# Kernel tuning notes

Measured on AMD Instinct MI355X. Metric: run time of the kernel, lower is better.

The kernel has to match this reference:

```python
import jax, jax.numpy as jnp
import numpy as np

EPS = 1e-08
LN_EPS = 1e-05


def _layernorm(x, g, b):
    mu = jnp.mean(x, axis=-1, keepdims=True)
    var = jnp.var(x, axis=-1, keepdims=True)
    return (x - mu) * jax.lax.rsqrt(var + LN_EPS) * g + b


def _prob(x):
    x = jnp.tanh(x) * 0.499 + 0.5
    return jnp.clip(x / (jnp.sum(x, axis=-1, keepdims=True) + EPS), EPS)


def setup_inputs() -> dict:
    key = jax.random.key(0)
    ks = jax.random.split(key, 8)
    B, N, D = 8, 2048, 1024
    H = 4 * D
    s = 0.02
    return {
        'q': jax.random.normal(ks[0], (B, N, D), jnp.float32),
        'k': jax.random.normal(ks[1], (B, N, D), jnp.float32),
        'v': jax.random.normal(ks[2], (B, N, D), jnp.float32),
        'W_diff': jax.random.normal(ks[3], (D, D), jnp.float32) * s,
        'b_diff': jnp.zeros((D,), jnp.float32),
        'ln_g': jnp.ones((D,), jnp.float32),
        'ln_b': jnp.zeros((D,), jnp.float32),
        'W1': jax.random.normal(ks[4], (H, D), jnp.float32) * s,
        'b1': jnp.zeros((H,), jnp.float32),
        'W2': jax.random.normal(ks[5], (D, H), jnp.float32) * s,
        'b2': jnp.zeros((D,), jnp.float32),
    }


def reference(q, k, v, W_diff, b_diff, ln_g, ln_b, W1, b1, W2, b2):
    D = q.shape[-1]
    q_prob = _prob(q)  # [B,N,D]
    k_prob = _prob(k)  # [B,N,D]
    log_ratio = jnp.log(q_prob) - jnp.log(k_prob)  # [B,N,D]
    # sid[b,i,j] = sum_d (q_prob[b,i,d] - k_prob[b,i,d]) * log_ratio[b,j,d]
    sid = jnp.einsum('bnd,bmd->bnm', q_prob - k_prob, log_ratio)
    sid_sim = -sid
    attn = jax.nn.softmax(sid_sim / (D ** 0.5), axis=-1)  # [B,N,N]
    attn_feat = jnp.einsum('bnm,bmd->bnd', attn, v)
    f_diff = (v - attn_feat) @ W_diff.T + b_diff + q
    h = _layernorm(f_diff, ln_g, ln_b)
    mlp = jax.nn.gelu(h @ W1.T + b1, approximate=False) @ W2.T + b2
    out = mlp + f_diff
    return _layernorm(out, ln_g, ln_b)
```

## Files before the change

### kernel.cpp

```cpp
#include <hip/hip_runtime.h>
#include <math.h>

typedef unsigned short u16;
typedef __attribute__((ext_vector_type(4))) unsigned short u16x4;
typedef __attribute__((ext_vector_type(8))) short s16x8;
typedef __attribute__((ext_vector_type(4))) float f32x4;
typedef __attribute__((ext_vector_type(4))) float f4v;

#define DEVI static __device__ __forceinline__

DEVI u16 f2bf(float f) {
  union { float f; unsigned u; } c; c.f = f;
  return (u16)((c.u + 0x7FFFu + ((c.u >> 16) & 1u)) >> 16);
}
DEVI float bf2f(u16 h) {
  union { unsigned u; float f; } c; c.u = ((unsigned)h) << 16;
  return c.f;
}
DEVI unsigned cvt_pk_bf16(float lo, float hi) {
  unsigned r;
  asm("v_cvt_pk_bf16_f32 %0, %1, %2" : "=v"(r) : "v"(lo), "v"(hi));
  return r;
}

DEVI float tanh_fast(float x) {
  float e = __expf(2.0f * x);
  float r = __builtin_amdgcn_rcpf(e + 1.0f);
  return fmaf(-2.0f, r, 1.0f);
}
DEVI float gelu_fast(float x) {
  float x2 = x * x;
  float u = x * fmaf(x2, 0.0356774081f, 0.7978845608f);
  float e = __expf(2.0f * u);
  float r = __builtin_amdgcn_rcpf(e + 1.0f);
  float t = fmaf(-2.0f, r, 1.0f);
  float hx = 0.5f * x;
  return fmaf(hx, t, hx);
}

DEVI void load_lds16(const u16* g, u16* l) {
  __builtin_amdgcn_global_load_lds(
      (const __attribute__((address_space(1))) void*)g,
      (__attribute__((address_space(3))) void*)l, 16, 0, 0);
}

#define BARL()                                                             \
  asm volatile("s_barrier\n\ts_waitcnt lgkmcnt(0)" ::: "memory");          \
  __builtin_amdgcn_sched_barrier(0)
#define BARL_VM4()                                                         \
  asm volatile("s_waitcnt vmcnt(4)\n\ts_barrier\n\ts_waitcnt lgkmcnt(0)" ::: "memory"); \
  __builtin_amdgcn_sched_barrier(0)
#define BARL_VM0()                                                         \
  asm volatile("s_waitcnt vmcnt(0)\n\ts_barrier\n\ts_waitcnt lgkmcnt(0)" ::: "memory"); \
  __builtin_amdgcn_sched_barrier(0)


__global__ __launch_bounds__(256) void cast3_kernel(
    const float* __restrict__ wd, const float* __restrict__ w1,
    const float* __restrict__ w2, u16* __restrict__ owd,
    u16* __restrict__ ow1, u16* __restrict__ ow2) {
  const int n1 = 262144, n2 = 1048576;
  int i = blockIdx.x * 256 + threadIdx.x;
  const float* src; u16* dst; int j;
  if (i < n1) { src = wd; dst = owd; j = i; }
  else if (i < n1 + n2) { src = w1; dst = ow1; j = i - n1; }
  else { src = w2; dst = ow2; j = i - n1 - n2; }
  f4v f = ((const f4v*)src)[j];
  u16x4 o;
  o[0] = f2bf(f[0]); o[1] = f2bf(f[1]); o[2] = f2bf(f[2]); o[3] = f2bf(f[3]);
  ((u16x4*)dst)[j] = o;
}

__global__ __launch_bounds__(256) void prob_kernel(
    const float* __restrict__ q, const float* __restrict__ k,
    u16* __restrict__ A, u16* __restrict__ Bm) {
  const int D = 1024;
  size_t row = blockIdx.x;
  int t = threadIdx.x;
  f4v qv = ((const f4v*)(q + row * D))[t];
  f4v kv = ((const f4v*)(k + row * D))[t];
  float tq[4], tk[4];
  float sq = 0.f, sk = 0.f;
#pragma unroll
  for (int i = 0; i < 4; i++) {
    tq[i] = tanh_fast(qv[i]) * 0.499f + 0.5f;
    tk[i] = tanh_fast(kv[i]) * 0.499f + 0.5f;
    sq += tq[i]; sk += tk[i];
  }
#pragma unroll
  for (int off = 32; off > 0; off >>= 1) {
    sq += __shfl_xor(sq, off);
    sk += __shfl_xor(sk, off);
  }
  __shared__ float sbq[4], sbk[4];
  int lane = t & 63, w = t >> 6;
  if (lane == 0) { sbq[w] = sq; sbk[w] = sk; }
  __syncthreads();
  sq = sbq[0] + sbq[1] + sbq[2] + sbq[3];
  sk = sbk[0] + sbk[1] + sbk[2] + sbk[3];
  float iq = 1.0f / (sq + 1e-8f), ik = 1.0f / (sk + 1e-8f);
  u16x4 av, bv;
#pragma unroll
  for (int i = 0; i < 4; i++) {
    float qp = fmaxf(tq[i] * iq, 1e-8f);
    float kp = fmaxf(tk[i] * ik, 1e-8f);
    av[i] = f2bf(qp - kp);
    bv[i] = f2bf(__logf(qp) - __logf(kp));
  }
  ((u16x4*)(A + row * D))[t] = av;
  ((u16x4*)(Bm + row * D))[t] = bv;
}

__global__ __launch_bounds__(256) void transpose_v_kernel(
    const float* __restrict__ v, u16* __restrict__ Vt) {
  const int N = 2048, D = 1024;
  __shared__ float tile[32][33];
  int b = blockIdx.z;
  int d0 = blockIdx.x * 32, n0 = blockIdx.y * 32;
  int tx = threadIdx.x & 31, ty = threadIdx.x >> 5;
  const float* vb = v + (size_t)b * N * D;
  u16* vtb = Vt + (size_t)b * N * D;
#pragma unroll
  for (int i = 0; i < 4; i++)
    tile[ty + i * 8][tx] = vb[(size_t)(n0 + ty + i * 8) * D + d0 + tx];
  __syncthreads();
#pragma unroll
  for (int i = 0; i < 4; i++)
    vtb[(size_t)(d0 + ty + i * 8) * N + n0 + tx] = f2bf(tile[tx][ty + i * 8]);
}

__global__ __launch_bounds__(256) void softmax_rows_kernel(u16* __restrict__ S) {
  const int NN = 2048;
  size_t row = blockIdx.x;
  u16* r = S + row * NN;
  int t = threadIdx.x;
  s16x8 vv = ((const s16x8*)r)[t];
  float x[8];
  float mx = -1e30f;
#pragma unroll
  for (int i = 0; i < 8; i++) { x[i] = bf2f((u16)vv[i]); mx = fmaxf(mx, x[i]); }
#pragma unroll
  for (int off = 32; off > 0; off >>= 1) mx = fmaxf(mx, __shfl_xor(mx, off));
  __shared__ float sm[4], ss[4];
  int lane = t & 63, w = t >> 6;
  if (lane == 0) sm[w] = mx;
  __syncthreads();
  mx = fmaxf(fmaxf(sm[0], sm[1]), fmaxf(sm[2], sm[3]));
  float sum = 0.f;
#pragma unroll
  for (int i = 0; i < 8; i++) { x[i] = __expf(x[i] - mx); sum += x[i]; }
#pragma unroll
  for (int off = 32; off > 0; off >>= 1) sum += __shfl_xor(sum, off);
  if (lane == 0) ss[w] = sum;
  __syncthreads();
  float inv = 1.0f / (ss[0] + ss[1] + ss[2] + ss[3]);
  s16x8 ov;
#pragma unroll
  for (int i = 0; i < 8; i++) ov[i] = (short)f2bf(x[i] * inv);
  ((s16x8*)r)[t] = ov;
}

template <int IN_BF16, int OUT_BF16>
__global__ __launch_bounds__(256) void layernorm_rows_kernel(
    const void* __restrict__ inp, void* __restrict__ outp,
    const float* __restrict__ g, const float* __restrict__ bia) {
  const int D = 1024;
  size_t row = blockIdx.x;
  int t = threadIdx.x;
  f4v xv;
  if (IN_BF16) {
    u16x4 h4 = ((const u16x4*)inp)[row * (D / 4) + t];
    xv[0] = bf2f(h4[0]); xv[1] = bf2f(h4[1]); xv[2] = bf2f(h4[2]); xv[3] = bf2f(h4[3]);
  } else {
    xv = ((const f4v*)inp)[row * (D / 4) + t];
  }
  float s = xv[0] + xv[1] + xv[2] + xv[3];
  float s2 = xv[0] * xv[0] + xv[1] * xv[1] + xv[2] * xv[2] + xv[3] * xv[3];
#pragma unroll
  for (int off = 32; off > 0; off >>= 1) {
    s += __shfl_xor(s, off);
    s2 += __shfl_xor(s2, off);
  }
  __shared__ float sa[4], sb[4];
  int lane = t & 63, w = t >> 6;
  if (lane == 0) { sa[w] = s; sb[w] = s2; }
  __syncthreads();
  s = sa[0] + sa[1] + sa[2] + sa[3];
  s2 = sb[0] + sb[1] + sb[2] + sb[3];
  float mean = s * (1.0f / D);
  float var = s2 * (1.0f / D) - mean * mean;
  float rs = rsqrtf(var + 1e-5f);
  f4v gv = ((const f4v*)g)[t];
  f4v bv = ((const f4v*)bia)[t];
  float y[4];
#pragma unroll
  for (int i = 0; i < 4; i++) y[i] = (xv[i] - mean) * rs * gv[i] + bv[i];
  if (OUT_BF16) {
    u16x4 o; o[0] = f2bf(y[0]); o[1] = f2bf(y[1]); o[2] = f2bf(y[2]); o[3] = f2bf(y[3]);
    ((u16x4*)outp)[row * (D / 4) + t] = o;
  } else {
    f4v o; o[0] = y[0]; o[1] = y[1]; o[2] = y[2]; o[3] = y[3];
    ((f4v*)outp)[row * (D / 4) + t] = o;
  }
}

template <int EPI>
__global__ __launch_bounds__(512, 2) void gemm8_kernel(
    const u16* __restrict__ Ab, const u16* __restrict__ Bb,
    void* __restrict__ Cout,
    const float* __restrict__ aux1, const float* __restrict__ aux2,
    int M, int Nc, int K,
    long sA, long sB, long sC, long sAux1, float scale) {
  __shared__ u16 lds[65536];

  int nwg = gridDim.x;
  int orig = blockIdx.x;
  int swz = (orig & 7) * (nwg >> 3) + (orig >> 3);
  int gxm = M >> 8, gyn = Nc >> 8;
  int pb = gxm * gyn;
  int bz = swz / pb;
  int rem = swz - bz * pb;
  int gsz = gyn << 3;
  int gid = rem / gsz;
  int lr = rem - gid * gsz;
  int bx = (gid << 3) + (lr & 7);
  int by = lr >> 3;
  int m0 = bx << 8, n0 = by << 8;

  const u16* Ap = Ab + (size_t)bz * sA;
  const u16* Bp = Bb + (size_t)bz * sB;

  int t = threadIdx.x, wid = t >> 6, l = t & 63;
  int wr = wid >> 2, wc = wid & 3;
  int sr = l >> 3;
  int scb = ((l & 7) ^ sr) * 8;
  int frow = l & 15, fq = l >> 4, fx = l & 7;

  const size_t rowoff = (size_t)(wid * 16 + sr) * K + scb;
  const u16* pA0 = Ap + (size_t)m0 * K + rowoff;
  const u16* pA0h = pA0 + (size_t)8 * K;
  const u16* pA1 = pA0 + (size_t)128 * K;
  const u16* pA1h = pA1 + (size_t)8 * K;
  const u16* pB0 = Bp + (size_t)n0 * K + rowoff;
  const u16* pB0h = pB0 + (size_t)8 * K;
  const u16* pB1 = pB0 + (size_t)128 * K;
  const u16* pB1h = pB1 + (size_t)8 * K;
  u16* ldA = &lds[wid * 1024];
  u16* ldB = ldA + 32768;

  int aoffs[4][2], boffs[2][2];
#pragma unroll
  for (int m = 0; m < 4; m++)
#pragma unroll
    for (int kk = 0; kk < 2; kk++)
      aoffs[m][kk] = ((wr * 64 + m * 16 + frow) * 64 + ((kk * 4 + fq) ^ fx) * 8) * 2;
#pragma unroll
  for (int n = 0; n < 2; n++)
#pragma unroll
    for (int kk = 0; kk < 2; kk++)
      boffs[n][kk] = ((wc * 32 + n * 16 + frow) * 64 + ((kk * 4 + fq) ^ fx) * 8) * 2 + 65536;

  s16x8 af[4][2], bf0[2][2], bf1[2][2];
  auto rdA = [&](int sl, int h) {
#pragma unroll
    for (int m = 0; m < 4; m++)
#pragma unroll
      for (int kk = 0; kk < 2; kk++)
        af[m][kk] = *(const s16x8*)((const char*)lds +
                                    (aoffs[m][kk] + (sl * 32768 + h * 16384)));
  };
  auto rdB = [&](int sl, int h, s16x8 (&bf)[2][2]) {
#pragma unroll
    for (int n = 0; n < 2; n++)
#pragma unroll
      for (int kk = 0; kk < 2; kk++)
        bf[n][kk] = *(const s16x8*)((const char*)lds +
                                    (boffs[n][kk] + (sl * 32768 + h * 16384)));
  };

  f32x4 acc[2][2][4][2];
#pragma unroll
  for (int a = 0; a < 2; a++)
#pragma unroll
    for (int b = 0; b < 2; b++)
#pragma unroll
      for (int m = 0; m < 4; m++)
#pragma unroll
        for (int n = 0; n < 2; n++) acc[a][b][m][n] = (f32x4){0.f, 0.f, 0.f, 0.f};

#define MFMA_Q(QM, QN, BF)                                                    \
  do {                                                                        \
    __builtin_amdgcn_s_setprio(1);                                            \
    _Pragma("unroll") for (int m = 0; m < 4; m++)                             \
        _Pragma("unroll") for (int n = 0; n < 2; n++)                         \
        _Pragma("unroll") for (int kk = 0; kk < 2; kk++)                      \
            acc[QM][QN][m][n] = __builtin_amdgcn_mfma_f32_16x16x32_bf16(      \
                af[m][kk], BF[n][kk], acc[QM][QN][m][n], 0, 0, 0);            \
    __builtin_amdgcn_s_setprio(0);                                            \
  } while (0)

  load_lds16(pA0, ldA);              load_lds16(pA0h, ldA + 512);
  load_lds16(pB1, ldB + 8192);       load_lds16(pB1h, ldB + 8192 + 512);
  load_lds16(pB0, ldB);              load_lds16(pB0h, ldB + 512);
  load_lds16(pA1, ldA + 8192);       load_lds16(pA1h, ldA + 8192 + 512);
  load_lds16(pA0 + 64, ldA + 16384); load_lds16(pA0h + 64, ldA + 16384 + 512);
  load_lds16(pB1 + 64, ldB + 16384 + 8192);
  load_lds16(pB1h + 64, ldB + 16384 + 8192 + 512);
  asm volatile("s_waitcnt vmcnt(4)\n\ts_barrier" ::: "memory");

  int nt = K >> 6, niter = nt >> 1;
  for (int i = 0; i < niter - 1; i++) {
    rdA(0, 0); rdB(0, 0, bf0);
    load_lds16(pB0 + 64, ldB + 16384);
    load_lds16(pB0h + 64, ldB + 16384 + 512);
    BARL(); MFMA_Q(0, 0, bf0);
    rdB(0, 1, bf1);
    load_lds16(pA1 + 64, ldA + 16384 + 8192);
    load_lds16(pA1h + 64, ldA + 16384 + 8192 + 512);
    BARL(); MFMA_Q(0, 1, bf1);
    rdA(0, 1);
    load_lds16(pA0 + 128, ldA);
    load_lds16(pA0h + 128, ldA + 512);
    BARL(); MFMA_Q(1, 1, bf1);
    load_lds16(pB1 + 128, ldB + 8192);
    load_lds16(pB1h + 128, ldB + 8192 + 512);
    BARL_VM4(); MFMA_Q(1, 0, bf0);
    rdA(1, 0); rdB(1, 0, bf0);
    load_lds16(pB0 + 128, ldB);
    load_lds16(pB0h + 128, ldB + 512);
    BARL(); MFMA_Q(0, 0, bf0);
    rdB(1, 1, bf1);
    load_lds16(pA1 + 128, ldA + 8192);
    load_lds16(pA1h + 128, ldA + 8192 + 512);
    BARL(); MFMA_Q(0, 1, bf1);
    rdA(1, 1);
    load_lds16(pA0 + 192, ldA + 16384);
    load_lds16(pA0h + 192, ldA + 16384 + 512);
    BARL(); MFMA_Q(1, 1, bf1);
    load_lds16(pB1 + 192, ldB + 16384 + 8192);
    load_lds16(pB1h + 192, ldB + 16384 + 8192 + 512);
    BARL_VM4(); MFMA_Q(1, 0, bf0);
    pA0 += 128; pA0h += 128; pA1 += 128; pA1h += 128;
    pB0 += 128; pB0h += 128; pB1 += 128; pB1h += 128;
  }
  {
    rdA(0, 0); rdB(0, 0, bf0);
    load_lds16(pB0 + 64, ldB + 16384);
    load_lds16(pB0h + 64, ldB + 16384 + 512);
    BARL(); MFMA_Q(0, 0, bf0);
    rdB(0, 1, bf1);
    load_lds16(pA1 + 64, ldA + 16384 + 8192);
    load_lds16(pA1h + 64, ldA + 16384 + 8192 + 512);
    BARL(); MFMA_Q(0, 1, bf1);
    rdA(0, 1);
    BARL(); MFMA_Q(1, 1, bf1);
    BARL_VM0(); MFMA_Q(1, 0, bf0);
    rdA(1, 0); rdB(1, 0, bf0);
    MFMA_Q(0, 0, bf0);
    rdB(1, 1, bf1);
    MFMA_Q(0, 1, bf1);
    rdA(1, 1);
    MFMA_Q(1, 1, bf1);
    MFMA_Q(1, 0, bf0);
  }
#undef MFMA_Q

#pragma unroll
  for (int qm = 0; qm < 2; qm++) {
#pragma unroll
    for (int qn = 0; qn < 2; qn++) {
#pragma unroll
      for (int m = 0; m < 4; m++) {
#pragma unroll
        for (int n = 0; n < 2; n++) {
          f32x4 a4 = acc[qm][qn][m][n];
          int gcol = n0 + qn * 128 + wc * 32 + n * 16 + frow;
#pragma unroll
          for (int rp = 0; rp < 2; rp++) {
            int grow0 = m0 + qm * 128 + wr * 64 + m * 16 + fq * 4 + rp * 2;
            size_t ci0 = (size_t)grow0 * Nc + gcol;
            if (EPI == 0) {
              unsigned pk = cvt_pk_bf16(a4[rp * 2] * scale, a4[rp * 2 + 1] * scale);
              ((u16*)Cout)[(size_t)bz * sC + ci0] = (u16)pk;
              ((u16*)Cout)[(size_t)bz * sC + ci0 + Nc] = (u16)(pk >> 16);
            } else if (EPI == 1) {
              float v0 = aux1[(size_t)bz * sAux1 + ci0];
              float v1 = aux1[(size_t)bz * sAux1 + ci0 + Nc];
              unsigned pk = cvt_pk_bf16(v0 - a4[rp * 2], v1 - a4[rp * 2 + 1]);
              ((u16*)Cout)[(size_t)bz * sC + ci0] = (u16)pk;
              ((u16*)Cout)[(size_t)bz * sC + ci0 + Nc] = (u16)(pk >> 16);
            } else if (EPI == 3) {
              float b2v = aux2[gcol];
              unsigned pk = cvt_pk_bf16(gelu_fast(a4[rp * 2] + b2v),
                                        gelu_fast(a4[rp * 2 + 1] + b2v));
              ((u16*)Cout)[ci0] = (u16)pk;
              ((u16*)Cout)[ci0 + Nc] = (u16)(pk >> 16);
            } else if (EPI == 6) {
              float b2v = aux2[gcol];
              unsigned pk = cvt_pk_bf16(a4[rp * 2] + b2v + aux1[ci0],
                                        a4[rp * 2 + 1] + b2v + aux1[ci0 + Nc]);
              ((u16*)Cout)[ci0] = (u16)pk;
              ((u16*)Cout)[ci0 + Nc] = (u16)(pk >> 16);
            } else {
              float b2v = aux2[gcol];
              const u16* r16 = (const u16*)aux1;
              unsigned pk = cvt_pk_bf16(a4[rp * 2] + b2v + bf2f(r16[ci0]),
                                        a4[rp * 2 + 1] + b2v + bf2f(r16[ci0 + Nc]));
              ((u16*)Cout)[ci0] = (u16)pk;
              ((u16*)Cout)[ci0 + Nc] = (u16)(pk >> 16);
            }
          }
        }
      }
    }
  }
}


extern "C" void kernel_launch(void* const* d_in, const int* in_sizes, int n_in,
                              void* d_out, int out_size, void* d_ws, size_t ws_size,
                              hipStream_t stream) {
  const float* q      = (const float*)d_in[0];
  const float* k      = (const float*)d_in[1];
  const float* v      = (const float*)d_in[2];
  const float* W_diff = (const float*)d_in[3];
  const float* b_diff = (const float*)d_in[4];
  const float* ln_g   = (const float*)d_in[5];
  const float* ln_b   = (const float*)d_in[6];
  const float* W1     = (const float*)d_in[7];
  const float* b1     = (const float*)d_in[8];
  const float* W2     = (const float*)d_in[9];
  const float* b2     = (const float*)d_in[10];

  const int B = 8, N = 2048, D = 1024, H = 4096;
  char* ws = (char*)d_ws;
  u16* A    = (u16*)(ws + 0);
  u16* Bm   = (u16*)(ws + 33554432);
  u16* X    = (u16*)(ws + 33554432);
  u16* Vt   = (u16*)(ws + 67108864);
  u16* S    = (u16*)(ws + 100663296);
  u16* Hbf  = (u16*)(ws + 134217728);
  u16* Wd   = (u16*)(ws + 167772160);
  u16* W1b  = (u16*)(ws + 169869312);
  u16* W2b  = (u16*)(ws + 178257920);
  u16* G    = (u16*)(ws + 0);
  u16* Fbf  = (u16*)d_out;
  float* out = (float*)d_out;

  cast3_kernel<<<9216, 256, 0, stream>>>(W_diff, W1, W2, Wd, W1b, W2b);

  prob_kernel<<<B * N, 256, 0, stream>>>(q, k, A, Bm);
  transpose_v_kernel<<<dim3(D / 32, N / 32, B), 256, 0, stream>>>(v, Vt);

  gemm8_kernel<0><<<8 * 8 * 8, 512, 0, stream>>>(
      A, Bm, S, nullptr, nullptr, N, N, D,
      (long)N * D, (long)N * D, (long)N * N, 0, -0.03125f);

  softmax_rows_kernel<<<B * N, 256, 0, stream>>>(S);

  gemm8_kernel<1><<<8 * 4 * 8, 512, 0, stream>>>(
      S, Vt, X, v, nullptr, N, D, N,
      (long)N * N, (long)D * N, (long)N * D, (long)N * D, 1.0f);

  gemm8_kernel<6><<<64 * 4, 512, 0, stream>>>(
      X, Wd, Fbf, q, b_diff, B * N, D, D, 0, 0, 0, 0, 1.0f);

  layernorm_rows_kernel<1, 1><<<B * N, 256, 0, stream>>>(Fbf, Hbf, ln_g, ln_b);

  gemm8_kernel<3><<<64 * 16, 512, 0, stream>>>(
      Hbf, W1b, G, nullptr, b1, B * N, H, D, 0, 0, 0, 0, 1.0f);

  gemm8_kernel<7><<<64 * 4, 512, 0, stream>>>(
      G, W2b, Hbf, (const float*)Fbf, b2, B * N, D, H, 0, 0, 0, 0, 1.0f);

  layernorm_rows_kernel<1, 0><<<B * N, 256, 0, stream>>>(Hbf, out, ln_g, ln_b);
}
```

Before: 552.4 us.

## Rework GEMM to 256x128 tiles with 3-stage K=32 LDS pipeline

Replaces the 256x256 tile, 128-K-step hand-scheduled quadrant pipeline with a 256x128 output tile and a three-slot ring buffer of K=32 stages. LDS use drops to about 72KB per block and launch bounds request four blocks per CU, with one barrier per K step. Grid sizes double to match. The aim is higher occupancy and simpler latency hiding. The cost is less operand reuse per tile (more global and LDS traffic per FLOP), plus more barriers per unit of work because each K step is shorter.

```diff
diff --git a/kernel.cpp b/kernel.cpp
--- a/kernel.cpp
+++ b/kernel.cpp
@@ -44,14 +44,10 @@
       (__attribute__((address_space(3))) void*)l, 16, 0, 0);
 }
 
-#define BARL()                                                             \
-  asm volatile("s_barrier\n\ts_waitcnt lgkmcnt(0)" ::: "memory");          \
-  __builtin_amdgcn_sched_barrier(0)
-#define BARL_VM4()                                                         \
-  asm volatile("s_waitcnt vmcnt(4)\n\ts_barrier\n\ts_waitcnt lgkmcnt(0)" ::: "memory"); \
-  __builtin_amdgcn_sched_barrier(0)
-#define BARL_VM0()                                                         \
-  asm volatile("s_waitcnt vmcnt(0)\n\ts_barrier\n\ts_waitcnt lgkmcnt(0)" ::: "memory"); \
+#define SYNC_VM3() asm volatile("s_waitcnt vmcnt(3)\n\ts_barrier" ::: "memory")
+#define SYNC_VM0() asm volatile("s_waitcnt vmcnt(0)\n\ts_barrier" ::: "memory")
+#define LGKM0()                                                \
+  asm volatile("s_waitcnt lgkmcnt(0)" ::: "memory");           \
   __builtin_amdgcn_sched_barrier(0)
 
 
@@ -205,18 +201,18 @@
 }
 
 template <int EPI>
-__global__ __launch_bounds__(512, 2) void gemm8_kernel(
+__global__ __launch_bounds__(512, 4) void gemm8_kernel(
     const u16* __restrict__ Ab, const u16* __restrict__ Bb,
     void* __restrict__ Cout,
     const float* __restrict__ aux1, const float* __restrict__ aux2,
     int M, int Nc, int K,
     long sA, long sB, long sC, long sAux1, float scale) {
-  __shared__ u16 lds[65536];
+  __shared__ u16 lds[36864];
 
   int nwg = gridDim.x;
   int orig = blockIdx.x;
   int swz = (orig & 7) * (nwg >> 3) + (orig >> 3);
-  int gxm = M >> 8, gyn = Nc >> 8;
+  int gxm = M >> 8, gyn = Nc >> 7;
   int pb = gxm * gyn;
   int bz = swz / pb;
   int rem = swz - bz * pb;
@@ -225,191 +221,134 @@
   int lr = rem - gid * gsz;
   int bx = (gid << 3) + (lr & 7);
   int by = lr >> 3;
-  int m0 = bx << 8, n0 = by << 8;
+  int m0 = bx << 8, n0 = by << 7;
 
   const u16* Ap = Ab + (size_t)bz * sA;
   const u16* Bp = Bb + (size_t)bz * sB;
 
   int t = threadIdx.x, wid = t >> 6, l = t & 63;
-  int wr = wid >> 2, wc = wid & 3;
-  int sr = l >> 3;
-  int scb = ((l & 7) ^ sr) * 8;
-  int frow = l & 15, fq = l >> 4, fx = l & 7;
-
-  const size_t rowoff = (size_t)(wid * 16 + sr) * K + scb;
-  const u16* pA0 = Ap + (size_t)m0 * K + rowoff;
-  const u16* pA0h = pA0 + (size_t)8 * K;
+  int wr = wid >> 1, wc = wid & 1;
+  int frow = l & 15, fq = l >> 4;
+
+  int srow = t >> 2;
+  int scg = ((t & 3) ^ ((t >> 3) & 3)) * 8;
+  const u16* pB  = Bp + ((size_t)n0 + srow) * K + scg;
+  const u16* pA0 = Ap + ((size_t)m0 + srow) * K + scg;
   const u16* pA1 = pA0 + (size_t)128 * K;
-  const u16* pA1h = pA1 + (size_t)8 * K;
-  const u16* pB0 = Bp + (size_t)n0 * K + rowoff;
-  const u16* pB0h = pB0 + (size_t)8 * K;
-  const u16* pB1 = pB0 + (size_t)128 * K;
-  const u16* pB1h = pB1 + (size_t)8 * K;
-  u16* ldA = &lds[wid * 1024];
-  u16* ldB = ldA + 32768;
-
-  int aoffs[4][2], boffs[2][2];
+
+  int aoffs[4], boffs[4];
+  int abase = (wr >> 1) * 8192;
+#pragma unroll
+  for (int m = 0; m < 4; m++) {
+    int rh = (wr & 1) * 64 + m * 16 + frow;
+    aoffs[m] = abase + rh * 64 + ((fq ^ ((rh >> 1) & 3)) * 16);
+  }
+#pragma unroll
+  for (int n = 0; n < 4; n++) {
+    int rb = wc * 64 + n * 16 + frow;
+    boffs[n] = 16384 + rb * 64 + ((fq ^ ((rb >> 1) & 3)) * 16);
+  }
+
+  s16x8 af[4], bf[4];
+  auto rdAB = [&](int slotB) {
+#pragma unroll
+    for (int m = 0; m < 4; m++)
+      af[m] = *(const s16x8*)((const char*)lds + (aoffs[m] + slotB));
+#pragma unroll
+    for (int n = 0; n < 4; n++)
+      bf[n] = *(const s16x8*)((const char*)lds + (boffs[n] + slotB));
+  };
+  auto stage = [&](int slotU16, const u16* b, const u16* a0, const u16* a1) {
+    load_lds16(b,  &lds[slotU16 + 8192 + t * 8]);
+    load_lds16(a0, &lds[slotU16 + t * 8]);
+    load_lds16(a1, &lds[slotU16 + 4096 + t * 8]);
+  };
+
+  f32x4 acc[4][4];
 #pragma unroll
   for (int m = 0; m < 4; m++)
 #pragma unroll
-    for (int kk = 0; kk < 2; kk++)
-      aoffs[m][kk] = ((wr * 64 + m * 16 + frow) * 64 + ((kk * 4 + fq) ^ fx) * 8) * 2;
-#pragma unroll
-  for (int n = 0; n < 2; n++)
-#pragma unroll
-    for (int kk = 0; kk < 2; kk++)
-      boffs[n][kk] = ((wc * 32 + n * 16 + frow) * 64 + ((kk * 4 + fq) ^ fx) * 8) * 2 + 65536;
-
-  s16x8 af[4][2], bf0[2][2], bf1[2][2];
-  auto rdA = [&](int sl, int h) {
-#pragma unroll
-    for (int m = 0; m < 4; m++)
-#pragma unroll
-      for (int kk = 0; kk < 2; kk++)
-        af[m][kk] = *(const s16x8*)((const char*)lds +
-                                    (aoffs[m][kk] + (sl * 32768 + h * 16384)));
-  };
-  auto rdB = [&](int sl, int h, s16x8 (&bf)[2][2]) {
-#pragma unroll
-    for (int n = 0; n < 2; n++)
-#pragma unroll
-      for (int kk = 0; kk < 2; kk++)
-        bf[n][kk] = *(const s16x8*)((const char*)lds +
-                                    (boffs[n][kk] + (sl * 32768 + h * 16384)));
-  };
-
-  f32x4 acc[2][2][4][2];
-#pragma unroll
-  for (int a = 0; a < 2; a++)
-#pragma unroll
-    for (int b = 0; b < 2; b++)
-#pragma unroll
-      for (int m = 0; m < 4; m++)
-#pragma unroll
-        for (int n = 0; n < 2; n++) acc[a][b][m][n] = (f32x4){0.f, 0.f, 0.f, 0.f};
-
-#define MFMA_Q(QM, QN, BF)                                                    \
+    for (int n = 0; n < 4; n++) acc[m][n] = (f32x4){0.f, 0.f, 0.f, 0.f};
+
+#define MFMA_ALL()                                                            \
   do {                                                                        \
     __builtin_amdgcn_s_setprio(1);                                            \
     _Pragma("unroll") for (int m = 0; m < 4; m++)                             \
-        _Pragma("unroll") for (int n = 0; n < 2; n++)                         \
-        _Pragma("unroll") for (int kk = 0; kk < 2; kk++)                      \
-            acc[QM][QN][m][n] = __builtin_amdgcn_mfma_f32_16x16x32_bf16(      \
-                af[m][kk], BF[n][kk], acc[QM][QN][m][n], 0, 0, 0);            \
+        _Pragma("unroll") for (int n = 0; n < 4; n++)                         \
+            acc[m][n] = __builtin_amdgcn_mfma_f32_16x16x32_bf16(              \
+                af[m], bf[n], acc[m][n], 0, 0, 0);                            \
     __builtin_amdgcn_s_setprio(0);                                            \
   } while (0)
 
-  load_lds16(pA0, ldA);              load_lds16(pA0h, ldA + 512);
-  load_lds16(pB1, ldB + 8192);       load_lds16(pB1h, ldB + 8192 + 512);
-  load_lds16(pB0, ldB);              load_lds16(pB0h, ldB + 512);
-  load_lds16(pA1, ldA + 8192);       load_lds16(pA1h, ldA + 8192 + 512);
-  load_lds16(pA0 + 64, ldA + 16384); load_lds16(pA0h + 64, ldA + 16384 + 512);
-  load_lds16(pB1 + 64, ldB + 16384 + 8192);
-  load_lds16(pB1h + 64, ldB + 16384 + 8192 + 512);
-  asm volatile("s_waitcnt vmcnt(4)\n\ts_barrier" ::: "memory");
-
-  int nt = K >> 6, niter = nt >> 1;
-  for (int i = 0; i < niter - 1; i++) {
-    rdA(0, 0); rdB(0, 0, bf0);
-    load_lds16(pB0 + 64, ldB + 16384);
-    load_lds16(pB0h + 64, ldB + 16384 + 512);
-    BARL(); MFMA_Q(0, 0, bf0);
-    rdB(0, 1, bf1);
-    load_lds16(pA1 + 64, ldA + 16384 + 8192);
-    load_lds16(pA1h + 64, ldA + 16384 + 8192 + 512);
-    BARL(); MFMA_Q(0, 1, bf1);
-    rdA(0, 1);
-    load_lds16(pA0 + 128, ldA);
-    load_lds16(pA0h + 128, ldA + 512);
-    BARL(); MFMA_Q(1, 1, bf1);
-    load_lds16(pB1 + 128, ldB + 8192);
-    load_lds16(pB1h + 128, ldB + 8192 + 512);
-    BARL_VM4(); MFMA_Q(1, 0, bf0);
-    rdA(1, 0); rdB(1, 0, bf0);
-    load_lds16(pB0 + 128, ldB);
-    load_lds16(pB0h + 128, ldB + 512);
-    BARL(); MFMA_Q(0, 0, bf0);
-    rdB(1, 1, bf1);
-    load_lds16(pA1 + 128, ldA + 8192);
-    load_lds16(pA1h + 128, ldA + 8192 + 512);
-    BARL(); MFMA_Q(0, 1, bf1);
-    rdA(1, 1);
-    load_lds16(pA0 + 192, ldA + 16384);
-    load_lds16(pA0h + 192, ldA + 16384 + 512);
-    BARL(); MFMA_Q(1, 1, bf1);
-    load_lds16(pB1 + 192, ldB + 16384 + 8192);
-    load_lds16(pB1h + 192, ldB + 16384 + 8192 + 512);
-    BARL_VM4(); MFMA_Q(1, 0, bf0);
-    pA0 += 128; pA0h += 128; pA1 += 128; pA1h += 128;
-    pB0 += 128; pB0h += 128; pB1 += 128; pB1h += 128;
-  }
-  {
-    rdA(0, 0); rdB(0, 0, bf0);
-    load_lds16(pB0 + 64, ldB + 16384);
-    load_lds16(pB0h + 64, ldB + 16384 + 512);
-    BARL(); MFMA_Q(0, 0, bf0);
-    rdB(0, 1, bf1);
-    load_lds16(pA1 + 64, ldA + 16384 + 8192);
-    load_lds16(pA1h + 64, ldA + 16384 + 8192 + 512);
-    BARL(); MFMA_Q(0, 1, bf1);
-    rdA(0, 1);
-    BARL(); MFMA_Q(1, 1, bf1);
-    BARL_VM0(); MFMA_Q(1, 0, bf0);
-    rdA(1, 0); rdB(1, 0, bf0);
-    MFMA_Q(0, 0, bf0);
-    rdB(1, 1, bf1);
-    MFMA_Q(0, 1, bf1);
-    rdA(1, 1);
-    MFMA_Q(1, 1, bf1);
-    MFMA_Q(1, 0, bf0);
-  }
-#undef MFMA_Q
-
-#pragma unroll
-  for (int qm = 0; qm < 2; qm++) {
-#pragma unroll
-    for (int qn = 0; qn < 2; qn++) {
-#pragma unroll
-      for (int m = 0; m < 4; m++) {
-#pragma unroll
-        for (int n = 0; n < 2; n++) {
-          f32x4 a4 = acc[qm][qn][m][n];
-          int gcol = n0 + qn * 128 + wc * 32 + n * 16 + frow;
-#pragma unroll
-          for (int rp = 0; rp < 2; rp++) {
-            int grow0 = m0 + qm * 128 + wr * 64 + m * 16 + fq * 4 + rp * 2;
-            size_t ci0 = (size_t)grow0 * Nc + gcol;
-            if (EPI == 0) {
-              unsigned pk = cvt_pk_bf16(a4[rp * 2] * scale, a4[rp * 2 + 1] * scale);
-              ((u16*)Cout)[(size_t)bz * sC + ci0] = (u16)pk;
-              ((u16*)Cout)[(size_t)bz * sC + ci0 + Nc] = (u16)(pk >> 16);
-            } else if (EPI == 1) {
-              float v0 = aux1[(size_t)bz * sAux1 + ci0];
-              float v1 = aux1[(size_t)bz * sAux1 + ci0 + Nc];
-              unsigned pk = cvt_pk_bf16(v0 - a4[rp * 2], v1 - a4[rp * 2 + 1]);
-              ((u16*)Cout)[(size_t)bz * sC + ci0] = (u16)pk;
-              ((u16*)Cout)[(size_t)bz * sC + ci0 + Nc] = (u16)(pk >> 16);
-            } else if (EPI == 3) {
-              float b2v = aux2[gcol];
-              unsigned pk = cvt_pk_bf16(gelu_fast(a4[rp * 2] + b2v),
-                                        gelu_fast(a4[rp * 2 + 1] + b2v));
-              ((u16*)Cout)[ci0] = (u16)pk;
-              ((u16*)Cout)[ci0 + Nc] = (u16)(pk >> 16);
-            } else if (EPI == 6) {
-              float b2v = aux2[gcol];
-              unsigned pk = cvt_pk_bf16(a4[rp * 2] + b2v + aux1[ci0],
-                                        a4[rp * 2 + 1] + b2v + aux1[ci0 + Nc]);
-              ((u16*)Cout)[ci0] = (u16)pk;
-              ((u16*)Cout)[ci0 + Nc] = (u16)(pk >> 16);
-            } else {
-              float b2v = aux2[gcol];
-              const u16* r16 = (const u16*)aux1;
-              unsigned pk = cvt_pk_bf16(a4[rp * 2] + b2v + bf2f(r16[ci0]),
-                                        a4[rp * 2 + 1] + b2v + bf2f(r16[ci0 + Nc]));
-              ((u16*)Cout)[ci0] = (u16)pk;
-              ((u16*)Cout)[ci0 + Nc] = (u16)(pk >> 16);
-            }
-          }
+  stage(0, pB, pA0, pA1);
+  stage(12288, pB + 32, pA0 + 32, pA1 + 32);
+
+  int nt = K >> 5;
+  int cur = 0;
+  int stg = 24576;
+  const u16* gB  = pB + 64;
+  const u16* gA0 = pA0 + 64;
+  const u16* gA1 = pA1 + 64;
+  for (int p = 0; p < nt - 2; p++) {
+    SYNC_VM3();
+    rdAB(cur * 2);
+    stage(stg, gB, gA0, gA1);
+    LGKM0();
+    MFMA_ALL();
+    gB += 32; gA0 += 32; gA1 += 32;
+    cur = (cur == 24576) ? 0 : cur + 12288;
+    stg = (stg == 24576) ? 0 : stg + 12288;
+  }
+  SYNC_VM3();
+  rdAB(cur * 2);
+  LGKM0();
+  MFMA_ALL();
+  cur = (cur == 24576) ? 0 : cur + 12288;
+  SYNC_VM0();
+  rdAB(cur * 2);
+  LGKM0();
+  MFMA_ALL();
+#undef MFMA_ALL
+
+#pragma unroll
+  for (int m = 0; m < 4; m++) {
+#pragma unroll
+    for (int n = 0; n < 4; n++) {
+      f32x4 a4 = acc[m][n];
+      int gcol = n0 + wc * 64 + n * 16 + frow;
+#pragma unroll
+      for (int rp = 0; rp < 2; rp++) {
+        int grow0 = m0 + wr * 64 + m * 16 + fq * 4 + rp * 2;
+        size_t ci0 = (size_t)grow0 * Nc + gcol;
+        if (EPI == 0) {
+          unsigned pk = cvt_pk_bf16(a4[rp * 2] * scale, a4[rp * 2 + 1] * scale);
+          ((u16*)Cout)[(size_t)bz * sC + ci0] = (u16)pk;
+          ((u16*)Cout)[(size_t)bz * sC + ci0 + Nc] = (u16)(pk >> 16);
+        } else if (EPI == 1) {
+          float v0 = aux1[(size_t)bz * sAux1 + ci0];
+          float v1 = aux1[(size_t)bz * sAux1 + ci0 + Nc];
+          unsigned pk = cvt_pk_bf16(v0 - a4[rp * 2], v1 - a4[rp * 2 + 1]);
+          ((u16*)Cout)[(size_t)bz * sC + ci0] = (u16)pk;
+          ((u16*)Cout)[(size_t)bz * sC + ci0 + Nc] = (u16)(pk >> 16);
+        } else if (EPI == 3) {
+          float b2v = aux2[gcol];
+          unsigned pk = cvt_pk_bf16(gelu_fast(a4[rp * 2] + b2v),
+                                    gelu_fast(a4[rp * 2 + 1] + b2v));
+          ((u16*)Cout)[ci0] = (u16)pk;
+          ((u16*)Cout)[ci0 + Nc] = (u16)(pk >> 16);
+        } else if (EPI == 6) {
+          float b2v = aux2[gcol];
+          unsigned pk = cvt_pk_bf16(a4[rp * 2] + b2v + aux1[ci0],
+                                    a4[rp * 2 + 1] + b2v + aux1[ci0 + Nc]);
+          ((u16*)Cout)[ci0] = (u16)pk;
+          ((u16*)Cout)[ci0 + Nc] = (u16)(pk >> 16);
+        } else {
+          float b2v = aux2[gcol];
+          const u16* r16 = (const u16*)aux1;
+          unsigned pk = cvt_pk_bf16(a4[rp * 2] + b2v + bf2f(r16[ci0]),
+                                    a4[rp * 2 + 1] + b2v + bf2f(r16[ci0 + Nc]));
+          ((u16*)Cout)[ci0] = (u16)pk;
+          ((u16*)Cout)[ci0 + Nc] = (u16)(pk >> 16);
         }
       }
     }
@@ -452,25 +391,25 @@
   prob_kernel<<<B * N, 256, 0, stream>>>(q, k, A, Bm);
   transpose_v_kernel<<<dim3(D / 32, N / 32, B), 256, 0, stream>>>(v, Vt);
 
-  gemm8_kernel<0><<<8 * 8 * 8, 512, 0, stream>>>(
+  gemm8_kernel<0><<<1024, 512, 0, stream>>>(
       A, Bm, S, nullptr, nullptr, N, N, D,
       (long)N * D, (long)N * D, (long)N * N, 0, -0.03125f);
 
   softmax_rows_kernel<<<B * N, 256, 0, stream>>>(S);
 
-  gemm8_kernel<1><<<8 * 4 * 8, 512, 0, stream>>>(
+  gemm8_kernel<1><<<512, 512, 0, stream>>>(
       S, Vt, X, v, nullptr, N, D, N,
       (long)N * N, (long)D * N, (long)N * D, (long)N * D, 1.0f);
 
-  gemm8_kernel<6><<<64 * 4, 512, 0, stream>>>(
+  gemm8_kernel<6><<<512, 512, 0, stream>>>(
       X, Wd, Fbf, q, b_diff, B * N, D, D, 0, 0, 0, 0, 1.0f);
 
   layernorm_rows_kernel<1, 1><<<B * N, 256, 0, stream>>>(Fbf, Hbf, ln_g, ln_b);
 
-  gemm8_kernel<3><<<64 * 16, 512, 0, stream>>>(
+  gemm8_kernel<3><<<2048, 512, 0, stream>>>(
       Hbf, W1b, G, nullptr, b1, B * N, H, D, 0, 0, 0, 0, 1.0f);
 
-  gemm8_kernel<7><<<64 * 4, 512, 0, stream>>>(
+  gemm8_kernel<7><<<512, 512, 0, stream>>>(
       G, W2b, Hbf, (const float*)Fbf, b2, B * N, D, H, 0, 0, 0, 0, 1.0f);
 
   layernorm_rows_kernel<1, 0><<<B * N, 256, 0, stream>>>(Hbf, out, ln_g, ln_b);
```

After: 627.3 us. 13.6% more time.
